# Optimization experiments

Hardware: AMD Instinct MI355X
Metric: run time of the kernel (lower is better)

The kernel has to match this reference:

```python
import jax, jax.numpy as jnp
import numpy as np

HIDDEN = 1024
NEG_INF = jnp.float32(-1e7)


def setup_inputs() -> dict:
    key = jax.random.key(0)
    ks = jax.random.split(key, 9)
    B, S, H = 4, 2048, HIDDEN
    std = 1.0 / np.sqrt(H)
    return {
        "queries": jax.random.normal(ks[0], (B, S, H), jnp.float32),
        "keys": jax.random.normal(ks[1], (B, S, H), jnp.float32),
        "values": jax.random.normal(ks[2], (B, S, H), jnp.float32),
        "Wq": jax.random.uniform(ks[3], (H, H), jnp.float32, -std, std),
        "bq": jax.random.uniform(ks[4], (H,), jnp.float32, -std, std),
        "Wk": jax.random.uniform(ks[5], (H, H), jnp.float32, -std, std),
        "bk": jax.random.uniform(ks[6], (H,), jnp.float32, -std, std),
        "Wv": jax.random.uniform(ks[7], (H, H), jnp.float32, -std, std),
        "bv": jax.random.uniform(ks[8], (H,), jnp.float32, -std, std),
    }


def reference(queries, keys, values, Wq, bq, Wk, bk, Wv, bv):
    # q,k,v: (B, S, H) linear projections (torch Linear: x @ W.T + b)
    q = jnp.einsum('bth,oh->bto', queries, Wq) + bq
    k = jnp.einsum('bsh,oh->bso', keys, Wk) + bk
    v = jnp.einsum('bsh,oh->bso', values, Wv) + bv
    scale = jax.lax.rsqrt(jnp.float32(q.shape[-1] * 0 + Wq.shape[0]))
    # scores[b, s, t] = <k_s, q_t> * scale   (key index s, query index t)
    scores = jnp.einsum('bsh,bth->bst', k, q) * scale
    S, T = scores.shape[1], scores.shape[2]
    # torch.tril(ones * -1e7, diagonal=-1): add -1e7 where s > t (strictly lower)
    mask = jnp.where(jnp.arange(S)[:, None] > jnp.arange(T)[None, :], NEG_INF, 0.0)
    attn = jax.nn.softmax(scores + mask, axis=1)  # softmax over key dim (dim=1)
    context = jnp.einsum('bst,bsh->bth', attn, v)  # (B, T, H)
    return context, attn
```

## Files before the change

kernel.cpp:

```cpp
#include <hip/hip_runtime.h>
#include <math.h>

typedef __bf16 bf16x8 __attribute__((ext_vector_type(8)));
typedef __bf16 bf16x4 __attribute__((ext_vector_type(4)));
typedef float f32x4 __attribute__((ext_vector_type(4)));

#define HD 1024
#define SEQ 2048
#define NB 4
#define WEL (HD * HD)

__device__ inline bf16x8 load8cvt(const __bf16* p) { return *(const bf16x8*)p; }
__device__ inline bf16x8 load8cvt(const float* p) {
    f32x4 a = *(const f32x4*)p;
    f32x4 b = *(const f32x4*)(p + 4);
    bf16x8 r;
#pragma unroll
    for (int i = 0; i < 4; ++i) { r[i] = (__bf16)a[i]; r[i + 4] = (__bf16)b[i]; }
    return r;
}

__device__ inline f32x4 load4f(const float* p) { return *(const f32x4*)p; }
__device__ inline f32x4 load4f(const __bf16* p) {
    bf16x4 v = *(const bf16x4*)p;
    f32x4 r;
#pragma unroll
    for (int i = 0; i < 4; ++i) r[i] = (float)v[i];
    return r;
}

__device__ inline void gld_lds16(const void* g, void* l) {
    __builtin_amdgcn_global_load_lds(
        (const __attribute__((address_space(1))) unsigned int*)g,
        (__attribute__((address_space(3))) unsigned int*)l, 16, 0, 0);
}

#define VMC(N) asm volatile("s_waitcnt vmcnt(" #N ")" ::: "memory")

template <typename T>
__device__ inline void stage_tile(const T* __restrict__ G, int ld, __bf16* s, int tid)
{
    const int r  = tid >> 3;
    const int co = ((tid & 7) ^ (r & 7)) * 8;
    if constexpr (sizeof(T) == 2) {
        __bf16* dst = s + (tid >> 6) * 512;
#pragma unroll
        for (int c = 0; c < 4; ++c)
            gld_lds16(G + (long)(c * 32 + r) * ld + co, dst + c * 2048);
    } else {
#pragma unroll
        for (int c = 0; c < 4; ++c)
            *(bf16x8*)(s + c * 2048 + tid * 8) = load8cvt(G + (long)(c * 32 + r) * ld + co);
    }
}

__device__ inline bf16x8 frag_read(const __bf16* s, int row, int c)
{
    return *(const bf16x8*)&s[row * 64 + ((c ^ (row & 7)) * 8)];
}

__device__ inline void mfma_ktile(const __bf16* __restrict__ sa,
                                  const __bf16* __restrict__ sb,
                                  int wm, int wn, int l15, int quad,
                                  f32x4 (&acc)[4][4])
{
#pragma unroll
    for (int kk = 0; kk < 64; kk += 32) {
        const int c8 = quad + (kk >> 3);
        bf16x8 af[4], bf[4];
#pragma unroll
        for (int i = 0; i < 4; ++i)
            af[i] = frag_read(sa, wm + i * 16 + l15, c8);
#pragma unroll
        for (int j = 0; j < 4; ++j)
            bf[j] = frag_read(sb, wn + j * 16 + l15, c8);
#pragma unroll
        for (int i = 0; i < 4; ++i)
#pragma unroll
            for (int j = 0; j < 4; ++j)
                acc[i][j] = __builtin_amdgcn_mfma_f32_16x16x32_bf16(af[i], bf[j], acc[i][j], 0, 0, 0);
    }
}

__device__ inline void stage32(const __bf16* __restrict__ G, int ld, __bf16* s, int tid)
{
    const int r = tid >> 2;
    const int c = ((tid & 3) ^ ((r >> 1) & 3)) * 8;
    __bf16* dst = s + (tid >> 6) * 512;
    gld_lds16(G + (long)r * ld + c, dst);
    gld_lds16(G + (long)(r + 64) * ld + c, dst + 2048);
}

__device__ __forceinline__ bf16x8 frag32(const __bf16* s, int row, int quad)
{
    return *(const bf16x8*)&s[row * 32 + ((quad ^ ((row >> 1) & 3)) * 8)];
}

struct Proj3 {
    const void* A[3];
    const void* W[3];
    const float* bias[3];
    __bf16* C[3];
    int vtmask;
};

__global__ __launch_bounds__(256) void gemm_proj_dp(Proj3 p)
{
    __shared__ __bf16 sA[4][128 * 32];
    __shared__ __bf16 sB[4][128 * 32];

    const int tid = threadIdx.x;
    const int L = blockIdx.x;
    const int per = gridDim.x >> 3;
    const int wrk = (L & 7) * per + (L >> 3);
    const int n0 = (wrk & 7) * 128;
    const int m0 = ((wrk >> 3) & 63) * 128;
    const int z  = wrk >> 9;
    const bool vt = (p.vtmask >> z) & 1;

    const __bf16* Ag = (const __bf16*)p.A[z] + (long)m0 * HD;
    const __bf16* Wg = (const __bf16*)p.W[z] + (long)n0 * HD;
    const float* bias = p.bias[z];
    __bf16* C = p.C[z];

    const int lane = tid & 63, l15 = lane & 15, quad = lane >> 4;
    const int wave = tid >> 6;
    const int wm = (wave >> 1) * 64;
    const int wn = (wave & 1) * 64;

    f32x4 acc[4][4];
    const f32x4 zero = {0.f, 0.f, 0.f, 0.f};
#pragma unroll
    for (int i = 0; i < 4; ++i)
#pragma unroll
        for (int j = 0; j < 4; ++j) acc[i][j] = zero;

    stage32(Ag,      HD, sA[0], tid); stage32(Wg,      HD, sB[0], tid);
    stage32(Ag + 32, HD, sA[1], tid); stage32(Wg + 32, HD, sB[1], tid);
    stage32(Ag + 64, HD, sA[2], tid); stage32(Wg + 64, HD, sB[2], tid);

    const int NT = HD / 32;
    for (int t = 0; t < NT; ++t) {
        if (t + 3 < NT) {
            stage32(Ag + (t + 3) * 32, HD, sA[(t + 3) & 3], tid);
            stage32(Wg + (t + 3) * 32, HD, sB[(t + 3) & 3], tid);
            VMC(12);
        } else if (t + 2 < NT) { VMC(8); }
        else if (t + 1 < NT)   { VMC(4); }
        else                   { VMC(0); }
        __builtin_amdgcn_s_barrier();
        __builtin_amdgcn_sched_barrier(0);
        const __bf16* sa = sA[t & 3];
        const __bf16* sb = sB[t & 3];
        bf16x8 af[4], bg[4];
#pragma unroll
        for (int i = 0; i < 4; ++i) af[i] = frag32(sa, wm + i * 16 + l15, quad);
#pragma unroll
        for (int j = 0; j < 4; ++j) bg[j] = frag32(sb, wn + j * 16 + l15, quad);
        __builtin_amdgcn_s_setprio(1);
#pragma unroll
        for (int i = 0; i < 4; ++i)
#pragma unroll
            for (int j = 0; j < 4; ++j)
                acc[i][j] = __builtin_amdgcn_mfma_f32_16x16x32_bf16(af[i], bg[j], acc[i][j], 0, 0, 0);
        __builtin_amdgcn_s_setprio(0);
        __builtin_amdgcn_s_barrier();
    }

#pragma unroll
    for (int j = 0; j < 4; ++j) {
        const int col = n0 + wn + j * 16 + l15;
        const float bv = bias[col];
#pragma unroll
        for (int i = 0; i < 4; ++i) {
#pragma unroll
            for (int r = 0; r < 4; ++r) {
                const int row = m0 + wm + i * 16 + quad * 4 + r;
                const float v = acc[i][j][r] + bv;
                if (vt) {
                    C[(((long)(row >> 11) * HD) + col) * SEQ + (row & (SEQ - 1))] = (__bf16)v;
                } else {
                    C[(long)row * HD + col] = (__bf16)v;
                }
            }
        }
    }
}

template <typename OutT>
__global__ __launch_bounds__(256) void gemm_sc(
    const __bf16* __restrict__ A, const __bf16* __restrict__ B,
    OutT* __restrict__ C, float* __restrict__ gsum, float alpha)
{
    __shared__ __bf16 s1[2][128 * 64];
    __shared__ __bf16 s2[2][128 * 64];
    __shared__ float csum[128];

    const int tid = threadIdx.x;
    const int L = blockIdx.x;
    const int per = gridDim.x >> 3;
    const int wrk = (L & 7) * per + (L >> 3);
    const int Lt = wrk % 136;
    const int z  = wrk / 136;
    int tb = (int)((sqrtf(8.f * Lt + 1.f) - 1.f) * 0.5f);
    while ((tb + 1) * (tb + 2) / 2 <= Lt) ++tb;
    while (tb * (tb + 1) / 2 > Lt) --tb;
    const int sb = Lt - tb * (tb + 1) / 2;
    const int m0 = tb * 128;
    const int n0 = sb * 128;

    const __bf16* Ag = A + (long)z * SEQ * HD + (long)m0 * HD;
    const __bf16* Bg = B + (long)z * SEQ * HD + (long)n0 * HD;
    C += (long)z * SEQ * SEQ;
    gsum += (long)z * SEQ;
    if (tid < 128) csum[tid] = 0.f;

    const int lane = tid & 63, l15 = lane & 15, quad = lane >> 4;
    const int wave = tid >> 6;
    const int wm = (wave >> 1) * 64;
    const int wn = (wave & 1) * 64;

    f32x4 acc[4][4];
    const f32x4 zero = {0.f, 0.f, 0.f, 0.f};
#pragma unroll
    for (int i = 0; i < 4; ++i)
#pragma unroll
        for (int j = 0; j < 4; ++j) acc[i][j] = zero;

    stage_tile(Ag, HD, s1[0], tid);
    stage_tile(Bg, HD, s2[0], tid);
    __syncthreads();
    int cur = 0;
    for (int kc = 0; kc < HD; kc += 64) {
        const int nxt = kc + 64;
        if (nxt < HD) {
            stage_tile(Ag + nxt, HD, s1[cur ^ 1], tid);
            stage_tile(Bg + nxt, HD, s2[cur ^ 1], tid);
        }
        mfma_ktile(s1[cur], s2[cur], wm, wn, l15, quad, acc);
        __syncthreads();
        cur ^= 1;
    }

    float rsum[4][4];
#pragma unroll
    for (int i = 0; i < 4; ++i)
#pragma unroll
        for (int r = 0; r < 4; ++r) rsum[i][r] = 0.f;

#pragma unroll
    for (int j = 0; j < 4; ++j) {
        const int col = n0 + wn + j * 16 + l15;
#pragma unroll
        for (int i = 0; i < 4; ++i) {
#pragma unroll
            for (int r = 0; r < 4; ++r) {
                const int row = m0 + wm + i * 16 + quad * 4 + r;
                const float e = (col <= row) ? __expf(acc[i][j][r] * alpha) : 0.f;
                C[(long)row * SEQ + col] = (OutT)e;
                rsum[i][r] += e;
            }
        }
    }
#pragma unroll
    for (int i = 0; i < 4; ++i) {
#pragma unroll
        for (int r = 0; r < 4; ++r) {
            float v = rsum[i][r];
            v += __shfl_xor(v, 1); v += __shfl_xor(v, 2);
            v += __shfl_xor(v, 4); v += __shfl_xor(v, 8);
            if (l15 == 0) atomicAdd(&csum[wm + i * 16 + quad * 4 + r], v);
        }
    }
    __syncthreads();
    if (tid < 128) atomicAdd(&gsum[m0 + tid], csum[tid]);
}

__global__ __launch_bounds__(256) void gemm_ctx(
    const __bf16* __restrict__ A, const __bf16* __restrict__ B,
    float* __restrict__ C, const float* __restrict__ gsum)
{
    __shared__ __bf16 s1[2][128 * 64];
    __shared__ __bf16 s2[2][128 * 64];
    __shared__ float rs[128];

    const int tid = threadIdx.x;
    const int L = blockIdx.x;
    const int per = gridDim.x >> 3;
    const int wrk = (L & 7) * per + (L >> 3);
    const int n0 = (wrk & 7) * 128;
    const int m0 = ((wrk >> 3) & 15) * 128;
    const int z  = wrk >> 7;

    const __bf16* Ag = A + (long)z * SEQ * SEQ + (long)m0 * SEQ;
    const __bf16* Bg = B + (long)z * HD * SEQ + (long)n0 * SEQ;
    C += (long)z * SEQ * HD;
    if (tid < 128) rs[tid] = gsum[(long)z * SEQ + m0 + tid];

    const int lane = tid & 63, l15 = lane & 15, quad = lane >> 4;
    const int wave = tid >> 6;
    const int wm = (wave >> 1) * 64;
    const int wn = (wave & 1) * 64;

    f32x4 acc[4][4];
    const f32x4 zero = {0.f, 0.f, 0.f, 0.f};
#pragma unroll
    for (int i = 0; i < 4; ++i)
#pragma unroll
        for (int j = 0; j < 4; ++j) acc[i][j] = zero;

    const int Kend = m0 + 128;

    stage_tile(Ag, SEQ, s1[0], tid);
    stage_tile(Bg, SEQ, s2[0], tid);
    __syncthreads();
    int cur = 0;
    for (int kc = 0; kc < Kend; kc += 64) {
        const int nxt = kc + 64;
        if (nxt < Kend) {
            stage_tile(Ag + nxt, SEQ, s1[cur ^ 1], tid);
            stage_tile(Bg + nxt, SEQ, s2[cur ^ 1], tid);
        }
        mfma_ktile(s1[cur], s2[cur], wm, wn, l15, quad, acc);
        __syncthreads();
        cur ^= 1;
    }

    float invr[4][4];
#pragma unroll
    for (int i = 0; i < 4; ++i)
#pragma unroll
        for (int r = 0; r < 4; ++r)
            invr[i][r] = 1.0f / rs[wm + i * 16 + quad * 4 + r];

#pragma unroll
    for (int j = 0; j < 4; ++j) {
        const int col = n0 + wn + j * 16 + l15;
#pragma unroll
        for (int i = 0; i < 4; ++i) {
#pragma unroll
            for (int r = 0; r < 4; ++r) {
                const int row = m0 + wm + i * 16 + quad * 4 + r;
                C[(long)row * HD + col] = acc[i][j][r] * invr[i][r];
            }
        }
    }
}

__global__ __launch_bounds__(256) void emit_attn(
    const __bf16* __restrict__ Et, float* __restrict__ Out,
    const float* __restrict__ csum)
{
    __shared__ float tile[64][65];
    const int b = blockIdx.z;
    const int t0 = blockIdx.x * 128;
    const int s0 = blockIdx.y * 128;
    const __bf16* Eb = Et + (long)b * SEQ * SEQ;
    float* Ob = Out + (long)b * SEQ * SEQ;
    const int tid = threadIdx.x;

    if (s0 > t0 + 127) {
        const f32x4 z4 = {0.f, 0.f, 0.f, 0.f};
        const int c4 = (tid & 31) * 4;
        for (int r = tid >> 5; r < 128; r += 8)
            *(f32x4*)&Ob[(long)(s0 + r) * SEQ + t0 + c4] = z4;
        return;
    }

#pragma unroll
    for (int dt = 0; dt < 2; ++dt) {
#pragma unroll
        for (int dsb = 0; dsb < 2; ++dsb) {
            const int tt = t0 + dt * 64, ss = s0 + dsb * 64;
            const int c4 = (tid & 15) * 4;
#pragma unroll
            for (int r0 = 0; r0 < 64; r0 += 16) {
                const int tl = r0 + (tid >> 4);
                const float inv = 1.0f / csum[(long)b * SEQ + tt + tl];
                f32x4 e = load4f(&Eb[(long)(tt + tl) * SEQ + ss + c4]);
#pragma unroll
                for (int k = 0; k < 4; ++k) tile[tl][c4 + k] = e[k] * inv;
            }
            __syncthreads();
            const int sl = tid >> 2;
            const int tc = (tid & 3) * 16;
            float v[16];
#pragma unroll
            for (int jj = 0; jj < 16; ++jj) v[jj] = tile[tc + jj][sl];
#pragma unroll
            for (int q = 0; q < 4; ++q) {
                f32x4 ov;
#pragma unroll
                for (int k = 0; k < 4; ++k) ov[k] = v[q * 4 + k];
                *(f32x4*)&Ob[(long)(ss + sl) * SEQ + tt + tc + q * 4] = ov;
            }
            __syncthreads();
        }
    }
}

template <bool TRI, bool CKLIM, bool EXPSUM, typename OutT>
__global__ __launch_bounds__(256) void gemm_bt(
    const __bf16* __restrict__ A, long strideA, int lda,
    const __bf16* __restrict__ B, long strideB, int ldb,
    OutT* __restrict__ C, long strideC, int ldc,
    float* __restrict__ gsum,
    int K, float alpha)
{
    __shared__ __bf16 sA[2][128 * 64];
    __shared__ __bf16 sB[2][128 * 64];
    __shared__ float csum[128];

    const int tid = threadIdx.x;
    const int L = blockIdx.x;
    const int per = gridDim.x >> 3;
    const int wrk = (L & 7) * per + (L >> 3);
    int n0, m0, z;
    if (TRI) {
        const int Lt = wrk % 136;
        z = wrk / 136;
        int tb = (int)((sqrtf(8.f * Lt + 1.f) - 1.f) * 0.5f);
        while ((tb + 1) * (tb + 2) / 2 <= Lt) ++tb;
        while (tb * (tb + 1) / 2 > Lt) --tb;
        const int sb = Lt - tb * (tb + 1) / 2;
        n0 = tb * 128;
        m0 = sb * 128;
    } else {
        n0 = (wrk & 7) * 128;
        m0 = ((wrk >> 3) & 15) * 128;
        z  = wrk >> 7;
    }

    const __bf16* Ag = A + (long)z * strideA + (long)m0 * lda;
    const __bf16* Bg = B + (long)z * strideB + (long)n0 * ldb;
    C += (long)z * strideC;
    if (EXPSUM) {
        gsum += (long)z * SEQ;
        if (tid < 128) csum[tid] = 0.f;
    }

    const int lane = tid & 63;
    const int l15  = lane & 15;
    const int quad = lane >> 4;
    const int wave = tid >> 6;
    const int wm = (wave >> 1) * 64;
    const int wn = (wave & 1) * 64;

    f32x4 acc[4][4];
    const f32x4 zero = {0.f, 0.f, 0.f, 0.f};
#pragma unroll
    for (int i = 0; i < 4; ++i)
#pragma unroll
        for (int j = 0; j < 4; ++j) acc[i][j] = zero;

    const int Kend = CKLIM ? min(K, m0 + 128) : K;

    stage_tile(Ag, lda, sA[0], tid);
    stage_tile(Bg, ldb, sB[0], tid);
    __syncthreads();

    int cur = 0;
    for (int kc = 0; kc < Kend; kc += 64) {
        const int nxt = kc + 64;
        if (nxt < Kend) {
            stage_tile(Ag + nxt, lda, sA[cur ^ 1], tid);
            stage_tile(Bg + nxt, ldb, sB[cur ^ 1], tid);
        }
        mfma_ktile(sA[cur], sB[cur], wm, wn, l15, quad, acc);
        __syncthreads();
        cur ^= 1;
    }

#pragma unroll
    for (int j = 0; j < 4; ++j) {
        const int col = n0 + wn + j * 16 + l15;
        float part = 0.f;
#pragma unroll
        for (int i = 0; i < 4; ++i) {
#pragma unroll
            for (int r = 0; r < 4; ++r) {
                const int row = m0 + wm + i * 16 + quad * 4 + r;
                float v = acc[i][j][r] * alpha;
                if (EXPSUM) {
                    v = __expf(v);
                    if (row <= col) part += v;
                }
                C[(long)row * ldc + col] = (OutT)v;
            }
        }
        if (EXPSUM) atomicAdd(&csum[wn + j * 16 + l15], part);
    }
    if (EXPSUM) {
        __syncthreads();
        if (tid < 128) atomicAdd(&gsum[n0 + tid], csum[tid]);
    }
}

template <typename TA, typename TW>
__global__ __launch_bounds__(256) void gemm_proj(Proj3 p)
{
    __shared__ __bf16 sA[2][128 * 64];
    __shared__ __bf16 sB[2][128 * 64];

    const int tid = threadIdx.x;
    const int L = blockIdx.x;
    const int per = gridDim.x >> 3;
    const int wrk = (L & 7) * per + (L >> 3);
    const int n0 = (wrk & 7) * 128;
    const int m0 = ((wrk >> 3) & 63) * 128;
    const int z  = wrk >> 9;
    const bool vt = (p.vtmask >> z) & 1;

    const TA* Ag = (const TA*)p.A[z] + (long)m0 * HD;
    const TW* Wg = (const TW*)p.W[z] + (long)n0 * HD;
    const float* bias = p.bias[z];
    __bf16* C = p.C[z];

    const int lane = tid & 63;
    const int l15  = lane & 15;
    const int quad = lane >> 4;
    const int wave = tid >> 6;
    const int wm = (wave >> 1) * 64;
    const int wn = (wave & 1) * 64;

    f32x4 acc[4][4];
    const f32x4 zero = {0.f, 0.f, 0.f, 0.f};
#pragma unroll
    for (int i = 0; i < 4; ++i)
#pragma unroll
        for (int j = 0; j < 4; ++j) acc[i][j] = zero;

    stage_tile(Ag, HD, sA[0], tid);
    stage_tile(Wg, HD, sB[0], tid);
    __syncthreads();

    int cur = 0;
    for (int kc = 0; kc < HD; kc += 64) {
        const int nxt = kc + 64;
        if (nxt < HD) {
            stage_tile(Ag + nxt, HD, sA[cur ^ 1], tid);
            stage_tile(Wg + nxt, HD, sB[cur ^ 1], tid);
        }
        mfma_ktile(sA[cur], sB[cur], wm, wn, l15, quad, acc);
        __syncthreads();
        cur ^= 1;
    }

#pragma unroll
    for (int j = 0; j < 4; ++j) {
        const int col = n0 + wn + j * 16 + l15;
        const float bv = bias[col];
#pragma unroll
        for (int i = 0; i < 4; ++i) {
#pragma unroll
            for (int r = 0; r < 4; ++r) {
                const int row = m0 + wm + i * 16 + quad * 4 + r;
                const float v = acc[i][j][r] + bv;
                if (vt) {
                    C[(((long)(row >> 11) * HD) + col) * SEQ + (row & (SEQ - 1))] = (__bf16)v;
                } else {
                    C[(long)row * HD + col] = (__bf16)v;
                }
            }
        }
    }
}

template <typename ET>
__global__ __launch_bounds__(256) void scale_emit(
    const ET* __restrict__ E, float* __restrict__ Out,
    const float* __restrict__ csum, __bf16* __restrict__ AT)
{
    __shared__ __bf16 tile[64][65];
    const int b = blockIdx.z;
    const int t0 = blockIdx.x * 128;
    const int s0 = blockIdx.y * 128;
    const ET* Eb = E + (long)b * SEQ * SEQ;
    float* Ob = Out + (long)b * SEQ * SEQ;
    __bf16* Ab = AT + (long)b * SEQ * SEQ;
    const int tid = threadIdx.x;

    if (s0 > t0 + 127) {
        const f32x4 z4 = {0.f, 0.f, 0.f, 0.f};
        const int c4 = (tid & 31) * 4;
        for (int r = tid >> 5; r < 128; r += 8)
            *(f32x4*)&Ob[(long)(s0 + r) * SEQ + t0 + c4] = z4;
        return;
    }

#pragma unroll
    for (int ds = 0; ds < 2; ++ds) {
#pragma unroll
        for (int dt = 0; dt < 2; ++dt) {
            const int ss = s0 + ds * 64, tt = t0 + dt * 64;
            const int c4 = (tid & 15) * 4;
            const int tcol = tt + c4;
            const f32x4 sv = *(const f32x4*)&csum[(long)b * SEQ + tcol];
            f32x4 inv;
#pragma unroll
            for (int k = 0; k < 4; ++k) inv[k] = 1.0f / sv[k];
#pragma unroll
            for (int r0 = 0; r0 < 64; r0 += 16) {
                const int s = ss + r0 + (tid >> 4);
                f32x4 e = load4f(&Eb[(long)s * SEQ + tcol]);
                f32x4 p;
#pragma unroll
                for (int k = 0; k < 4; ++k)
                    p[k] = (s <= tcol + k) ? e[k] * inv[k] : 0.f;
                *(f32x4*)&Ob[(long)s * SEQ + tcol] = p;
#pragma unroll
                for (int k = 0; k < 4; ++k)
                    tile[r0 + (tid >> 4)][c4 + k] = (__bf16)p[k];
            }
            __syncthreads();
            const int tr = tid >> 2;
            const int sc = (tid & 3) * 16;
            __bf16 v[16];
#pragma unroll
            for (int jj = 0; jj < 16; ++jj) v[jj] = tile[sc + jj][tr];
            *(bf16x8*)&Ab[(long)(tt + tr) * SEQ + ss + sc]     = *(bf16x8*)v;
            *(bf16x8*)&Ab[(long)(tt + tr) * SEQ + ss + sc + 8] = *(bf16x8*)(v + 8);
            __syncthreads();
        }
    }
}

struct CvtJob { const float* in; __bf16* out; int nblk; };
struct Cvt6 { CvtJob j[6]; };
__global__ __launch_bounds__(256) void cvt_bf16(Cvt6 c)
{
    const CvtJob jb = c.j[blockIdx.y];
    if ((int)blockIdx.x >= jb.nblk) return;
    const long i = ((long)blockIdx.x * 256 + threadIdx.x) * 8;
    *(bf16x8*)&jb.out[i] = load8cvt(&jb.in[i]);
}

extern "C" void kernel_launch(void* const* d_in, const int* in_sizes, int n_in,
                              void* d_out, int out_size, void* d_ws, size_t ws_size,
                              hipStream_t stream)
{
    const float* queries = (const float*)d_in[0];
    const float* keys    = (const float*)d_in[1];
    const float* values  = (const float*)d_in[2];
    const float* Wq = (const float*)d_in[3];
    const float* bq = (const float*)d_in[4];
    const float* Wk = (const float*)d_in[5];
    const float* bk = (const float*)d_in[6];
    const float* Wv = (const float*)d_in[7];
    const float* bv = (const float*)d_in[8];

    const long tokens = (long)NB * SEQ;
    const long pe = tokens * HD;
    const size_t SLOT = (size_t)pe * sizeof(__bf16);
    const int ABLK = (int)(pe / 2048);
    const int WBLK = WEL / 2048;

    float* outCtx  = (float*)d_out;
    float* outAttn = outCtx + tokens * HD;
    __bf16* wb = (__bf16*)outAttn;
    __bf16* Wqb = wb, *Wkb = wb + WEL, *Wvb = wb + 2 * WEL;

    const dim3 blk(256);
    char* w = (char*)d_ws;
    __bf16 *qp, *kp, *vT;

    if (ws_size >= 6 * SLOT) {
        __bf16* xq = (__bf16*)w;
        __bf16* xk = (__bf16*)(w + SLOT);
        __bf16* xv = (__bf16*)(w + 2 * SLOT);
        qp = (__bf16*)(w + 3 * SLOT);
        kp = (__bf16*)(w + 4 * SLOT);
        vT = (__bf16*)(w + 5 * SLOT);
        __bf16* Ebf = (__bf16*)w;
        float* colsum = (float*)(w + 2 * SLOT);

        Cvt6 cv = {{{queries, xq, ABLK}, {keys, xk, ABLK}, {values, xv, ABLK},
                    {Wq, Wqb, WBLK}, {Wk, Wkb, WBLK}, {Wv, Wvb, WBLK}}};
        cvt_bf16<<<dim3(ABLK, 6), blk, 0, stream>>>(cv);
        Proj3 pj = {{xq, xk, xv}, {Wqb, Wkb, Wvb}, {bq, bk, bv}, {qp, kp, vT}, 4};
        gemm_proj_dp<<<dim3(512 * 3), blk, 0, stream>>>(pj);

        hipMemsetAsync(colsum, 0, (size_t)NB * SEQ * sizeof(float), stream);
        gemm_sc<__bf16><<<dim3(544), blk, 0, stream>>>(qp, kp, Ebf, colsum, 0.03125f);
        emit_attn<<<dim3(SEQ / 128, SEQ / 128, NB), blk, 0, stream>>>(
            Ebf, outAttn, colsum);
        gemm_ctx<<<dim3(512), blk, 0, stream>>>(Ebf, vT, outCtx, colsum);
    } else if (ws_size >= 4 * SLOT) {
        float* colsum = outCtx;
        hipMemsetAsync(colsum, 0, (size_t)NB * SEQ * sizeof(float), stream);
        __bf16* x0 = (__bf16*)w;
        qp = (__bf16*)(w + SLOT);
        kp = (__bf16*)(w + 2 * SLOT);
        __bf16* x1 = (__bf16*)(w + 3 * SLOT);
        vT = x1;
        __bf16* attnT = (__bf16*)d_ws;

        Cvt6 cv = {{{queries, x0, ABLK}, {keys, x1, ABLK},
                    {Wq, Wqb, WBLK}, {Wk, Wkb, WBLK}, {Wv, Wvb, WBLK},
                    {nullptr, nullptr, 0}}};
        cvt_bf16<<<dim3(ABLK, 5), blk, 0, stream>>>(cv);
        Proj3 pqk = {{x0, x1, nullptr}, {Wqb, Wkb, nullptr}, {bq, bk, nullptr},
                     {qp, kp, nullptr}, 0};
        gemm_proj_dp<<<dim3(512 * 2), blk, 0, stream>>>(pqk);
        Cvt6 cvv = {{{values, x0, ABLK}, {nullptr, nullptr, 0}, {nullptr, nullptr, 0},
                     {nullptr, nullptr, 0}, {nullptr, nullptr, 0}, {nullptr, nullptr, 0}}};
        cvt_bf16<<<dim3(ABLK, 1), blk, 0, stream>>>(cvv);
        Proj3 pv = {{x0, nullptr, nullptr}, {Wvb, nullptr, nullptr},
                    {bv, nullptr, nullptr}, {vT, nullptr, nullptr}, 1};
        gemm_proj_dp<<<dim3(512), blk, 0, stream>>>(pv);

        gemm_bt<true, false, true, float><<<dim3(544), blk, 0, stream>>>(
            kp, (long)SEQ * HD, HD, qp, (long)SEQ * HD, HD,
            outAttn, (long)SEQ * SEQ, SEQ, colsum, HD, 0.03125f);
        scale_emit<float><<<dim3(SEQ / 128, SEQ / 128, NB), blk, 0, stream>>>(
            outAttn, outAttn, colsum, attnT);
        gemm_bt<false, true, false, float><<<dim3(512), blk, 0, stream>>>(
            attnT, (long)SEQ * SEQ, SEQ, vT, (long)HD * SEQ, SEQ,
            outCtx, (long)SEQ * HD, HD, nullptr, SEQ, 1.0f);
    } else {
        float* colsum = outCtx;
        hipMemsetAsync(colsum, 0, (size_t)NB * SEQ * sizeof(float), stream);
        qp = (__bf16*)w;
        kp = (__bf16*)(w + SLOT);
        vT = (__bf16*)(w + 2 * SLOT);
        __bf16* attnT = (__bf16*)d_ws;
        Proj3 pj = {{queries, keys, values}, {Wq, Wk, Wv}, {bq, bk, bv},
                    {qp, kp, vT}, 4};
        gemm_proj<float, float><<<dim3(512 * 3), blk, 0, stream>>>(pj);

        gemm_bt<true, false, true, float><<<dim3(544), blk, 0, stream>>>(
            kp, (long)SEQ * HD, HD, qp, (long)SEQ * HD, HD,
            outAttn, (long)SEQ * SEQ, SEQ, colsum, HD, 0.03125f);
        scale_emit<float><<<dim3(SEQ / 128, SEQ / 128, NB), blk, 0, stream>>>(
            outAttn, outAttn, colsum, attnT);
        gemm_bt<false, true, false, float><<<dim3(512), blk, 0, stream>>>(
            attnT, (long)SEQ * SEQ, SEQ, vT, (long)HD * SEQ, SEQ,
            outCtx, (long)SEQ * HD, HD, nullptr, SEQ, 1.0f);
    }
}
```

Measured before the change: 399.5 us.

## Revert projection GEMM to double-buffered, reorder ctx m-blocks, adjust emit tile padding

Drops the 4-stage, 32-wide K pipeline projection kernel with explicit vmcnt waits and brings back the simpler double-buffered 64-wide K-tile gemm_proj template. The context GEMM now interleaves m-block order, pairing light and heavy rows of the triangular attention matrix so per-block work is spread more evenly. The emit kernel's transpose tile padding changes from 65 to 68 and its readback is restructured to read the shared tile per output vector instead of caching 16 values in registers. Each part shifts the balance between latency hiding, load balance and shared-memory bank conflicts.

```diff
diff --git a/kernel.cpp b/kernel.cpp
--- a/kernel.cpp
+++ b/kernel.cpp
@@ -35,8 +35,6 @@
         (__attribute__((address_space(3))) unsigned int*)l, 16, 0, 0);
 }
 
-#define VMC(N) asm volatile("s_waitcnt vmcnt(" #N ")" ::: "memory")
-
 template <typename T>
 __device__ inline void stage_tile(const T* __restrict__ G, int ld, __bf16* s, int tid)
 {
@@ -80,20 +78,6 @@
             for (int j = 0; j < 4; ++j)
                 acc[i][j] = __builtin_amdgcn_mfma_f32_16x16x32_bf16(af[i], bf[j], acc[i][j], 0, 0, 0);
     }
-}
-
-__device__ inline void stage32(const __bf16* __restrict__ G, int ld, __bf16* s, int tid)
-{
-    const int r = tid >> 2;
-    const int c = ((tid & 3) ^ ((r >> 1) & 3)) * 8;
-    __bf16* dst = s + (tid >> 6) * 512;
-    gld_lds16(G + (long)r * ld + c, dst);
-    gld_lds16(G + (long)(r + 64) * ld + c, dst + 2048);
-}
-
-__device__ __forceinline__ bf16x8 frag32(const __bf16* s, int row, int quad)
-{
-    return *(const bf16x8*)&s[row * 32 + ((quad ^ ((row >> 1) & 3)) * 8)];
 }
 
 struct Proj3 {
@@ -104,10 +88,11 @@
     int vtmask;
 };
 
-__global__ __launch_bounds__(256) void gemm_proj_dp(Proj3 p)
-{
-    __shared__ __bf16 sA[4][128 * 32];
-    __shared__ __bf16 sB[4][128 * 32];
+template <typename TA, typename TW>
+__global__ __launch_bounds__(256) void gemm_proj(Proj3 p)
+{
+    __shared__ __bf16 sA[2][128 * 64];
+    __shared__ __bf16 sB[2][128 * 64];
 
     const int tid = threadIdx.x;
     const int L = blockIdx.x;
@@ -118,12 +103,14 @@
     const int z  = wrk >> 9;
     const bool vt = (p.vtmask >> z) & 1;
 
-    const __bf16* Ag = (const __bf16*)p.A[z] + (long)m0 * HD;
-    const __bf16* Wg = (const __bf16*)p.W[z] + (long)n0 * HD;
+    const TA* Ag = (const TA*)p.A[z] + (long)m0 * HD;
+    const TW* Wg = (const TW*)p.W[z] + (long)n0 * HD;
     const float* bias = p.bias[z];
     __bf16* C = p.C[z];
 
-    const int lane = tid & 63, l15 = lane & 15, quad = lane >> 4;
+    const int lane = tid & 63;
+    const int l15  = lane & 15;
+    const int quad = lane >> 4;
     const int wave = tid >> 6;
     const int wm = (wave >> 1) * 64;
     const int wn = (wave & 1) * 64;
@@ -135,36 +122,20 @@
 #pragma unroll
         for (int j = 0; j < 4; ++j) acc[i][j] = zero;
 
-    stage32(Ag,      HD, sA[0], tid); stage32(Wg,      HD, sB[0], tid);
-    stage32(Ag + 32, HD, sA[1], tid); stage32(Wg + 32, HD, sB[1], tid);
-    stage32(Ag + 64, HD, sA[2], tid); stage32(Wg + 64, HD, sB[2], tid);
-
-    const int NT = HD / 32;
-    for (int t = 0; t < NT; ++t) {
-        if (t + 3 < NT) {
-            stage32(Ag + (t + 3) * 32, HD, sA[(t + 3) & 3], tid);
-            stage32(Wg + (t + 3) * 32, HD, sB[(t + 3) & 3], tid);
-            VMC(12);
-        } else if (t + 2 < NT) { VMC(8); }
-        else if (t + 1 < NT)   { VMC(4); }
-        else                   { VMC(0); }
-        __builtin_amdgcn_s_barrier();
-        __builtin_amdgcn_sched_barrier(0);
-        const __bf16* sa = sA[t & 3];
-        const __bf16* sb = sB[t & 3];
-        bf16x8 af[4], bg[4];
-#pragma unroll
-        for (int i = 0; i < 4; ++i) af[i] = frag32(sa, wm + i * 16 + l15, quad);
-#pragma unroll
-        for (int j = 0; j < 4; ++j) bg[j] = frag32(sb, wn + j * 16 + l15, quad);
-        __builtin_amdgcn_s_setprio(1);
-#pragma unroll
-        for (int i = 0; i < 4; ++i)
-#pragma unroll
-            for (int j = 0; j < 4; ++j)
-                acc[i][j] = __builtin_amdgcn_mfma_f32_16x16x32_bf16(af[i], bg[j], acc[i][j], 0, 0, 0);
-        __builtin_amdgcn_s_setprio(0);
-        __builtin_amdgcn_s_barrier();
+    stage_tile(Ag, HD, sA[0], tid);
+    stage_tile(Wg, HD, sB[0], tid);
+    __syncthreads();
+
+    int cur = 0;
+    for (int kc = 0; kc < HD; kc += 64) {
+        const int nxt = kc + 64;
+        if (nxt < HD) {
+            stage_tile(Ag + nxt, HD, sA[cur ^ 1], tid);
+            stage_tile(Wg + nxt, HD, sB[cur ^ 1], tid);
+        }
+        mfma_ktile(sA[cur], sB[cur], wm, wn, l15, quad, acc);
+        __syncthreads();
+        cur ^= 1;
     }
 
 #pragma unroll
@@ -289,7 +260,9 @@
     const int per = gridDim.x >> 3;
     const int wrk = (L & 7) * per + (L >> 3);
     const int n0 = (wrk & 7) * 128;
-    const int m0 = ((wrk >> 3) & 15) * 128;
+    const int q  = (wrk >> 3) & 15;
+    const int mb = (q & 1) ? (15 - (q >> 1)) : (q >> 1);
+    const int m0 = mb * 128;
     const int z  = wrk >> 7;
 
     const __bf16* Ag = A + (long)z * SEQ * SEQ + (long)m0 * SEQ;
@@ -351,7 +324,7 @@
     const __bf16* __restrict__ Et, float* __restrict__ Out,
     const float* __restrict__ csum)
 {
-    __shared__ float tile[64][65];
+    __shared__ float tile[64][68];
     const int b = blockIdx.z;
     const int t0 = blockIdx.x * 128;
     const int s0 = blockIdx.y * 128;
@@ -383,16 +356,13 @@
             }
             __syncthreads();
             const int sl = tid >> 2;
-            const int tc = (tid & 3) * 16;
-            float v[16];
-#pragma unroll
-            for (int jj = 0; jj < 16; ++jj) v[jj] = tile[tc + jj][sl];
-#pragma unroll
-            for (int q = 0; q < 4; ++q) {
+            const int t4 = (tid & 3) * 4;
+#pragma unroll
+            for (int qq = 0; qq < 4; ++qq) {
                 f32x4 ov;
 #pragma unroll
-                for (int k = 0; k < 4; ++k) ov[k] = v[q * 4 + k];
-                *(f32x4*)&Ob[(long)(ss + sl) * SEQ + tt + tc + q * 4] = ov;
+                for (int k = 0; k < 4; ++k) ov[k] = tile[qq * 16 + t4 + k][sl];
+                *(f32x4*)&Ob[(long)(ss + sl) * SEQ + tt + qq * 16 + t4] = ov;
             }
             __syncthreads();
         }
@@ -496,76 +466,6 @@
     }
 }
 
-template <typename TA, typename TW>
-__global__ __launch_bounds__(256) void gemm_proj(Proj3 p)
-{
-    __shared__ __bf16 sA[2][128 * 64];
-    __shared__ __bf16 sB[2][128 * 64];
-
-    const int tid = threadIdx.x;
-    const int L = blockIdx.x;
-    const int per = gridDim.x >> 3;
-    const int wrk = (L & 7) * per + (L >> 3);
-    const int n0 = (wrk & 7) * 128;
-    const int m0 = ((wrk >> 3) & 63) * 128;
-    const int z  = wrk >> 9;
-    const bool vt = (p.vtmask >> z) & 1;
-
-    const TA* Ag = (const TA*)p.A[z] + (long)m0 * HD;
-    const TW* Wg = (const TW*)p.W[z] + (long)n0 * HD;
-    const float* bias = p.bias[z];
-    __bf16* C = p.C[z];
-
-    const int lane = tid & 63;
-    const int l15  = lane & 15;
-    const int quad = lane >> 4;
-    const int wave = tid >> 6;
-    const int wm = (wave >> 1) * 64;
-    const int wn = (wave & 1) * 64;
-
-    f32x4 acc[4][4];
-    const f32x4 zero = {0.f, 0.f, 0.f, 0.f};
-#pragma unroll
-    for (int i = 0; i < 4; ++i)
-#pragma unroll
-        for (int j = 0; j < 4; ++j) acc[i][j] = zero;
-
-    stage_tile(Ag, HD, sA[0], tid);
-    stage_tile(Wg, HD, sB[0], tid);
-    __syncthreads();
-
-    int cur = 0;
-    for (int kc = 0; kc < HD; kc += 64) {
-        const int nxt = kc + 64;
-        if (nxt < HD) {
-            stage_tile(Ag + nxt, HD, sA[cur ^ 1], tid);
-            stage_tile(Wg + nxt, HD, sB[cur ^ 1], tid);
-        }
-        mfma_ktile(sA[cur], sB[cur], wm, wn, l15, quad, acc);
-        __syncthreads();
-        cur ^= 1;
-    }
-
-#pragma unroll
-    for (int j = 0; j < 4; ++j) {
-        const int col = n0 + wn + j * 16 + l15;
-        const float bv = bias[col];
-#pragma unroll
-        for (int i = 0; i < 4; ++i) {
-#pragma unroll
-            for (int r = 0; r < 4; ++r) {
-                const int row = m0 + wm + i * 16 + quad * 4 + r;
-                const float v = acc[i][j][r] + bv;
-                if (vt) {
-                    C[(((long)(row >> 11) * HD) + col) * SEQ + (row & (SEQ - 1))] = (__bf16)v;
-                } else {
-                    C[(long)row * HD + col] = (__bf16)v;
-                }
-            }
-        }
-    }
-}
-
 template <typename ET>
 __global__ __launch_bounds__(256) void scale_emit(
     const ET* __restrict__ E, float* __restrict__ Out,
@@ -678,7 +578,7 @@
                     {Wq, Wqb, WBLK}, {Wk, Wkb, WBLK}, {Wv, Wvb, WBLK}}};
         cvt_bf16<<<dim3(ABLK, 6), blk, 0, stream>>>(cv);
         Proj3 pj = {{xq, xk, xv}, {Wqb, Wkb, Wvb}, {bq, bk, bv}, {qp, kp, vT}, 4};
-        gemm_proj_dp<<<dim3(512 * 3), blk, 0, stream>>>(pj);
+        gemm_proj<__bf16, __bf16><<<dim3(512 * 3), blk, 0, stream>>>(pj);
 
         hipMemsetAsync(colsum, 0, (size_t)NB * SEQ * sizeof(float), stream);
         gemm_sc<__bf16><<<dim3(544), blk, 0, stream>>>(qp, kp, Ebf, colsum, 0.03125f);
@@ -701,13 +601,13 @@
         cvt_bf16<<<dim3(ABLK, 5), blk, 0, stream>>>(cv);
         Proj3 pqk = {{x0, x1, nullptr}, {Wqb, Wkb, nullptr}, {bq, bk, nullptr},
                      {qp, kp, nullptr}, 0};
-        gemm_proj_dp<<<dim3(512 * 2), blk, 0, stream>>>(pqk);
+        gemm_proj<__bf16, __bf16><<<dim3(512 * 2), blk, 0, stream>>>(pqk);
         Cvt6 cvv = {{{values, x0, ABLK}, {nullptr, nullptr, 0}, {nullptr, nullptr, 0},
                      {nullptr, nullptr, 0}, {nullptr, nullptr, 0}, {nullptr, nullptr, 0}}};
         cvt_bf16<<<dim3(ABLK, 1), blk, 0, stream>>>(cvv);
         Proj3 pv = {{x0, nullptr, nullptr}, {Wvb, nullptr, nullptr},
                     {bv, nullptr, nullptr}, {vT, nullptr, nullptr}, 1};
-        gemm_proj_dp<<<dim3(512), blk, 0, stream>>>(pv);
+        gemm_proj<__bf16, __bf16><<<dim3(512), blk, 0, stream>>>(pv);
 
         gemm_bt<true, false, true, float><<<dim3(544), blk, 0, stream>>>(
             kp, (long)SEQ * HD, HD, qp, (long)SEQ * HD, HD,
```

Result: faster. 376.6 us (-5.7%).
